# Kernel optimization log

Hardware: AMD Instinct MI355X
Metric: run time of the kernel (lower is better)

The kernel has to match this reference:

```python
import jax, jax.numpy as jnp
import numpy as np

B, H = 1048576, 128

def setup_inputs() -> dict:
    key = jax.random.key(0)
    ks = jax.random.split(key, 7)
    return {
        "x": jax.random.normal(ks[0], (B, 2), dtype=jnp.float32),
        "W1": jax.random.normal(ks[1], (1, H), dtype=jnp.float32) * 0.1,
        "b1": jax.random.normal(ks[2], (H,), dtype=jnp.float32) * 0.1,
        "W2": jax.random.normal(ks[3], (H, H), dtype=jnp.float32) * 0.05,
        "b2": jax.random.normal(ks[4], (H,), dtype=jnp.float32) * 0.1,
        "W3": jax.random.normal(ks[5], (H, 2), dtype=jnp.float32) * 0.01,
        "b3": jax.random.normal(ks[6], (2,), dtype=jnp.float32) * 0.01,
    }

def reference(x, W1, b1, W2, b2, W3, b3):
    # mask_type = 0, inverse = False
    z_id = x[:, 0:1]   # [B, 1]
    z_tr = x[:, 1:2]   # [B, 1]
    h = jax.nn.relu(z_id @ W1 + b1)          # [B, H]
    h = jax.nn.relu(h @ W2 + b2)             # [B, H]
    st = h @ W3 + b3                          # [B, 2]
    s = jnp.tanh(st[:, 0:1])
    t = st[:, 1:2]
    z_tr_out = z_tr * jnp.exp(s) + t
    return jnp.concatenate([z_id, z_tr_out], axis=1)
```

## Files before the change

kernel.cpp:

```cpp
#include <hip/hip_runtime.h>
#include <hip/hip_bf16.h>


#define TABN 512
#define ZLO  (-8.0f)
#define ZHI  ( 8.0f)

typedef float f32x4 __attribute__((ext_vector_type(4)));

__global__ __launch_bounds__(64) void build_table_kernel(
    const float* __restrict__ W1, const float* __restrict__ b1,
    const float* __restrict__ W2, const float* __restrict__ b2,
    const float* __restrict__ W3, const float* __restrict__ b3,
    float4* __restrict__ tab4)
{
    const int lane = threadIdx.x;
    const int base = blockIdx.x * 2;
    const float hstep = (ZHI - ZLO) / (float)TABN;

    const float w1a = W1[lane],      b1a = b1[lane];
    const float w1b = W1[lane + 64], b1b = b1[lane + 64];
    const float bb2a = b2[lane], bb2b = b2[lane + 64];

    float h1a[3], h1b[3], accA[3], accB[3];
    #pragma unroll
    for (int p = 0; p < 3; ++p) {
        const float z = ZLO + (float)(base + p) * hstep;
        h1a[p] = fmaxf(fmaf(z, w1a, b1a), 0.0f);
        h1b[p] = fmaxf(fmaf(z, w1b, b1b), 0.0f);
        accA[p] = bb2a;
        accB[p] = bb2b;
    }

    #pragma unroll 8
    for (int k = 0; k < 64; ++k) {
        const float w20 = W2[k * 128 + lane];
        const float w21 = W2[k * 128 + lane + 64];
        #pragma unroll
        for (int p = 0; p < 3; ++p) {
            const float hk = __shfl(h1a[p], k);
            accA[p] = fmaf(hk, w20, accA[p]);
            accB[p] = fmaf(hk, w21, accB[p]);
        }
    }
    #pragma unroll 8
    for (int k = 0; k < 64; ++k) {
        const float w20 = W2[(k + 64) * 128 + lane];
        const float w21 = W2[(k + 64) * 128 + lane + 64];
        #pragma unroll
        for (int p = 0; p < 3; ++p) {
            const float hk = __shfl(h1b[p], k);
            accA[p] = fmaf(hk, w20, accA[p]);
            accB[p] = fmaf(hk, w21, accB[p]);
        }
    }

    const float w30a = W3[2 * lane + 0],        w31a = W3[2 * lane + 1];
    const float w30b = W3[2 * (lane + 64) + 0], w31b = W3[2 * (lane + 64) + 1];

    float st0[3], st1[3];
    #pragma unroll
    for (int p = 0; p < 3; ++p) {
        const float h2a = fmaxf(accA[p], 0.0f);
        const float h2b = fmaxf(accB[p], 0.0f);
        float s0 = fmaf(h2a, w30a, h2b * w30b);
        float s1 = fmaf(h2a, w31a, h2b * w31b);
        #pragma unroll
        for (int off = 32; off; off >>= 1) {
            s0 += __shfl_xor(s0, off);
            s1 += __shfl_xor(s1, off);
        }
        st0[p] = s0; st1[p] = s1;
    }

    if (lane < 3) {
        const float myE = expf(tanhf(st0[lane] + b3[0]));
        const float myT = st1[lane] + b3[1];
        const float eN = __shfl(myE, lane + 1);
        const float tN = __shfl(myT, lane + 1);
        if (lane < 2)
            tab4[base + lane] = make_float4(eN - myE, tN - myT, myE, myT);
    }
}

__device__ __forceinline__ float couple_one(float zid, float ztr,
                                             const float4* __restrict__ tab4)
{
    const float inv_h = (float)TABN / (ZHI - ZLO);
    float u = fmaxf((zid - ZLO) * inv_h, 0.0f);
    int i0 = (int)u;
    i0 = min(i0, TABN - 1);
    const float f = u - (float)i0;
    const float4 s = tab4[i0];
    const float es = fmaf(f, s.x, s.z);
    const float t  = fmaf(f, s.y, s.w);
    return fmaf(ztr, es, t);
}

__global__ __launch_bounds__(256) void apply_kernel(
    const f32x4* __restrict__ x,
    const float4* __restrict__ tab4,
    f32x4* __restrict__ out,
    int n4, int odd)
{
    const int i = blockIdx.x * blockDim.x + threadIdx.x;
    if (i < n4) {
        const f32x4 v = __builtin_nontemporal_load(&x[i]);
        f32x4 o;
        o.x = v.x;
        o.y = couple_one(v.x, v.y, tab4);
        o.z = v.z;
        o.w = couple_one(v.z, v.w, tab4);
        __builtin_nontemporal_store(o, &out[i]);
    } else if (odd && i == n4) {
        const float2* x2 = (const float2*)x;
        float2* o2 = (float2*)out;
        const float2 v = x2[2 * n4];
        o2[2 * n4] = make_float2(v.x, couple_one(v.x, v.y, tab4));
    }
}

extern "C" void kernel_launch(void* const* d_in, const int* in_sizes, int n_in,
                              void* d_out, int out_size, void* d_ws, size_t ws_size,
                              hipStream_t stream)
{
    const float* W1 = (const float*)d_in[1];
    const float* b1 = (const float*)d_in[2];
    const float* W2 = (const float*)d_in[3];
    const float* b2 = (const float*)d_in[4];
    const float* W3 = (const float*)d_in[5];
    const float* b3 = (const float*)d_in[6];

    const int B = in_sizes[0] / 2;
    float4* tab4 = (float4*)d_ws;

    build_table_kernel<<<TABN / 2, 64, 0, stream>>>(W1, b1, W2, b2, W3, b3, tab4);

    const int n4  = B / 2;
    const int odd = B & 1;
    const int threads = 256;
    const int blocks  = (n4 + odd + threads - 1) / threads;
    apply_kernel<<<blocks, threads, 0, stream>>>(
        (const f32x4*)d_in[0], tab4, (f32x4*)d_out, n4, odd);
}
```

Baseline: 15.03 us.

## Split table-build K reduction across four waves with LDS partial sums

The table-building kernel now launches 256 threads per block, and each of the four waves handles a 32-row slice of the 128-long W2 reduction. Partial sums are combined through shared memory, then two waves apply ReLU and the W3 projection, and a final cross-wave sum produces the table entries. This is meant to shorten the serial latency of the small table-build kernel that runs before the apply pass. In exchange it adds shared-memory traffic and two block barriers.

```diff
diff --git a/kernel.cpp b/kernel.cpp
--- a/kernel.cpp
+++ b/kernel.cpp
@@ -8,78 +8,95 @@
 
 typedef float f32x4 __attribute__((ext_vector_type(4)));
 
-__global__ __launch_bounds__(64) void build_table_kernel(
+__global__ __launch_bounds__(256) void build_table_kernel(
     const float* __restrict__ W1, const float* __restrict__ b1,
     const float* __restrict__ W2, const float* __restrict__ b2,
     const float* __restrict__ W3, const float* __restrict__ b3,
     float4* __restrict__ tab4)
 {
-    const int lane = threadIdx.x;
+    __shared__ float part[4][3][128];
+    __shared__ float wsum[2][6];
+
+    const int tid  = threadIdx.x;
+    const int lane = tid & 63;
+    const int wave = tid >> 6;
     const int base = blockIdx.x * 2;
     const float hstep = (ZHI - ZLO) / (float)TABN;
 
-    const float w1a = W1[lane],      b1a = b1[lane];
-    const float w1b = W1[lane + 64], b1b = b1[lane + 64];
-    const float bb2a = b2[lane], bb2b = b2[lane + 64];
+    const int half  = wave >> 1;
+    const int kbase = (wave & 1) * 32;
+    const float w1  = W1[half * 64 + lane];
+    const float bb1 = b1[half * 64 + lane];
 
-    float h1a[3], h1b[3], accA[3], accB[3];
+    float hsrc[3], accA[3], accB[3];
     #pragma unroll
     for (int p = 0; p < 3; ++p) {
         const float z = ZLO + (float)(base + p) * hstep;
-        h1a[p] = fmaxf(fmaf(z, w1a, b1a), 0.0f);
-        h1b[p] = fmaxf(fmaf(z, w1b, b1b), 0.0f);
-        accA[p] = bb2a;
-        accB[p] = bb2b;
+        hsrc[p] = fmaxf(fmaf(z, w1, bb1), 0.0f);
+        accA[p] = 0.0f;
+        accB[p] = 0.0f;
     }
 
     #pragma unroll 8
-    for (int k = 0; k < 64; ++k) {
+    for (int kk = 0; kk < 32; ++kk) {
+        const int k = wave * 32 + kk;
         const float w20 = W2[k * 128 + lane];
         const float w21 = W2[k * 128 + lane + 64];
         #pragma unroll
         for (int p = 0; p < 3; ++p) {
-            const float hk = __shfl(h1a[p], k);
+            const float hk = __shfl(hsrc[p], kbase + kk);
             accA[p] = fmaf(hk, w20, accA[p]);
             accB[p] = fmaf(hk, w21, accB[p]);
         }
     }
-    #pragma unroll 8
-    for (int k = 0; k < 64; ++k) {
-        const float w20 = W2[(k + 64) * 128 + lane];
-        const float w21 = W2[(k + 64) * 128 + lane + 64];
+    #pragma unroll
+    for (int p = 0; p < 3; ++p) {
+        part[wave][p][lane]      = accA[p];
+        part[wave][p][lane + 64] = accB[p];
+    }
+    __syncthreads();
+
+    if (tid < 128) {
+        const int j = tid;
+        const float bb2 = b2[j];
+        const float w30 = W3[2 * j + 0];
+        const float w31 = W3[2 * j + 1];
+        float r0[3], r1[3];
         #pragma unroll
         for (int p = 0; p < 3; ++p) {
-            const float hk = __shfl(h1b[p], k);
-            accA[p] = fmaf(hk, w20, accA[p]);
-            accB[p] = fmaf(hk, w21, accB[p]);
+            float a = bb2 + ((part[0][p][j] + part[1][p][j]) +
+                             (part[2][p][j] + part[3][p][j]));
+            a = fmaxf(a, 0.0f);
+            r0[p] = a * w30;
+            r1[p] = a * w31;
+        }
+        #pragma unroll
+        for (int off = 32; off; off >>= 1) {
+            #pragma unroll
+            for (int p = 0; p < 3; ++p) {
+                r0[p] += __shfl_xor(r0[p], off);
+                r1[p] += __shfl_xor(r1[p], off);
+            }
+        }
+        if (lane == 0) {
+            #pragma unroll
+            for (int p = 0; p < 3; ++p) {
+                wsum[wave][p * 2 + 0] = r0[p];
+                wsum[wave][p * 2 + 1] = r1[p];
+            }
         }
     }
+    __syncthreads();
 
-    const float w30a = W3[2 * lane + 0],        w31a = W3[2 * lane + 1];
-    const float w30b = W3[2 * (lane + 64) + 0], w31b = W3[2 * (lane + 64) + 1];
-
-    float st0[3], st1[3];
-    #pragma unroll
-    for (int p = 0; p < 3; ++p) {
-        const float h2a = fmaxf(accA[p], 0.0f);
-        const float h2b = fmaxf(accB[p], 0.0f);
-        float s0 = fmaf(h2a, w30a, h2b * w30b);
-        float s1 = fmaf(h2a, w31a, h2b * w31b);
-        #pragma unroll
-        for (int off = 32; off; off >>= 1) {
-            s0 += __shfl_xor(s0, off);
-            s1 += __shfl_xor(s1, off);
-        }
-        st0[p] = s0; st1[p] = s1;
-    }
-
-    if (lane < 3) {
-        const float myE = expf(tanhf(st0[lane] + b3[0]));
-        const float myT = st1[lane] + b3[1];
-        const float eN = __shfl(myE, lane + 1);
-        const float tN = __shfl(myT, lane + 1);
-        if (lane < 2)
-            tab4[base + lane] = make_float4(eN - myE, tN - myT, myE, myT);
+    if (tid < 3) {
+        const float st0 = wsum[0][tid * 2 + 0] + wsum[1][tid * 2 + 0] + b3[0];
+        const float st1 = wsum[0][tid * 2 + 1] + wsum[1][tid * 2 + 1] + b3[1];
+        const float e = expf(tanhf(st0));
+        const float t = st1;
+        const float eN = __shfl(e, tid + 1);
+        const float tN = __shfl(t, tid + 1);
+        if (tid < 2)
+            tab4[base + tid] = make_float4(eN - e, tN - t, e, t);
     }
 }
 
@@ -134,7 +151,7 @@
     const int B = in_sizes[0] / 2;
     float4* tab4 = (float4*)d_ws;
 
-    build_table_kernel<<<TABN / 2, 64, 0, stream>>>(W1, b1, W2, b2, W3, b3, tab4);
+    build_table_kernel<<<TABN / 2, 256, 0, stream>>>(W1, b1, W2, b2, W3, b3, tab4);
 
     const int n4  = B / 2;
     const int odd = B & 1;
```

New measurement: 13.12 us. 12.7% less time.
